# Optimization experiments

Measured on AMD Instinct MI355X. Metric: run time of the kernel, lower is better.

## Reference

```python
import jax, jax.numpy as jnp
import numpy as np

DIM = 512
HIDDEN = 4 * DIM
B, N = 512, 81
EPS = 1e-5


def _act_quant(x):
    # per-token int8 absmax quantization (BitNet b1.58)
    scale = 127.0 / jnp.clip(jnp.max(jnp.abs(x), axis=-1, keepdims=True), EPS, None)
    q = jnp.clip(jnp.round(x * scale), -128.0, 127.0) / scale
    return x + jax.lax.stop_gradient(q - x)  # STE


def _weight_quant(w):
    # per-tensor ternary quantization with mean-|w| scale
    scale = 1.0 / jnp.clip(jnp.mean(jnp.abs(w)), EPS, None)
    q = jnp.clip(jnp.round(w * scale), -1.0, 1.0) / scale
    return w + jax.lax.stop_gradient(q - w)  # STE


def bitlinear(x, w):
    # x: [..., in], w: [out, in] (torch Linear layout), no bias
    return _act_quant(x) @ _weight_quant(w).T


def setup_inputs() -> dict:
    key = jax.random.key(0)
    ks = jax.random.split(key, 8)
    def p(k, shape, fan_in):
        return jax.random.normal(k, shape, dtype=jnp.float32) * (fan_in ** -0.5)
    return {
        "x": jax.random.normal(ks[0], (B, N, DIM), dtype=jnp.float32),
        "y": jax.random.normal(ks[1], (B, N, DIM), dtype=jnp.float32),
        "s_prev": jax.random.normal(ks[2], (B, N, DIM), dtype=jnp.float32),
        "W_in": p(ks[3], (DIM, 3 * DIM), 3 * DIM),
        "W_fc1": p(ks[4], (HIDDEN, DIM), DIM),
        "W_fc2": p(ks[5], (DIM, HIDDEN), HIDDEN),
        "W_z": p(ks[6], (DIM, DIM), DIM),
        "W_mask": p(ks[7], (1, DIM), DIM),
    }


def reference(x, y, s_prev, W_in, W_fc1, W_fc2, W_z, W_mask):
    # inner: proj_in(cat) then residual BitMLP block(s)
    h = bitlinear(jnp.concatenate([x, y, s_prev], axis=-1), W_in)  # [B,N,DIM]
    h = h + bitlinear(jax.nn.gelu(bitlinear(h, W_fc1), approximate=False), W_fc2)
    # emit
    z = bitlinear(h, W_z)                      # [B,N,DIM]
    focus_mask = jax.nn.sigmoid(bitlinear(h, W_mask))  # [B,N,1]
    return (z, focus_mask)
```

## Files before the change

kernel.cpp:

```cpp
#include <hip/hip_runtime.h>
#include <math.h>

typedef unsigned short u16;
typedef unsigned int u32;
typedef __attribute__((ext_vector_type(8))) short short8;
typedef __attribute__((ext_vector_type(4))) float f32x4;

#define EPSQ 1e-5f
#define B_ROWS 41472
#define Z_ELEMS ((size_t)B_ROWS * 512)

__device__ __forceinline__ u16 f2b(float f) {
  u32 x = __float_as_uint(f);
  u32 r = (x + 0x7fffu + ((x >> 16) & 1u)) >> 16;
  return (u16)r;
}
__device__ __forceinline__ float blo(u32 v) { return __uint_as_float(v << 16); }
__device__ __forceinline__ float bhi(u32 v) { return __uint_as_float(v & 0xffff0000u); }
__device__ __forceinline__ u32 pack2(float a, float b) {
  return (u32)f2b(a) | ((u32)f2b(b) << 16);
}

__device__ __forceinline__ float wredMax(float v) {
#pragma unroll
  for (int off = 32; off; off >>= 1) v = fmaxf(v, __shfl_xor(v, off));
  return v;
}
__device__ __forceinline__ float wredSum(float v) {
#pragma unroll
  for (int off = 32; off; off >>= 1) v += __shfl_xor(v, off);
  return v;
}

__global__ __launch_bounds__(256) void wq_sum(const float* __restrict__ w, int n,
                                              float* __restrict__ sum) {
  float acc = 0.f;
  for (int i = blockIdx.x * blockDim.x + threadIdx.x; i < n; i += gridDim.x * blockDim.x)
    acc += fabsf(w[i]);
  acc = wredSum(acc);
  if ((threadIdx.x & 63) == 0) atomicAdd(sum, acc);
}

__global__ __launch_bounds__(256) void wq_quant(const float* __restrict__ w, int n,
                                                const float* __restrict__ sum,
                                                float* __restrict__ mout,
                                                u16* __restrict__ q) {
  const float m = fmaxf(sum[0] / (float)n, EPSQ);
  if (blockIdx.x == 0 && threadIdx.x == 0) mout[0] = m;
  const float s = 1.0f / m;
  for (int i = blockIdx.x * blockDim.x + threadIdx.x; i < n; i += gridDim.x * blockDim.x) {
    float t = rintf(w[i] * s);
    t = fminf(fmaxf(t, -1.f), 1.f);
    q[i] = f2b(t);
  }
}

__global__ __launch_bounds__(256) void aq_concat(const float* __restrict__ x,
                                                 const float* __restrict__ y,
                                                 const float* __restrict__ s,
                                                 u16* __restrict__ qx,
                                                 float* __restrict__ dsc, int row0) {
  const int r = blockIdx.x;
  const size_t R = (size_t)(row0 + r);
  const int t = threadIdx.x;
  float2 vx = *(const float2*)(x + R * 512 + t * 2);
  float2 vy = *(const float2*)(y + R * 512 + t * 2);
  float2 vs = *(const float2*)(s + R * 512 + t * 2);
  float mx = fmaxf(fmaxf(fabsf(vx.x), fabsf(vx.y)),
                   fmaxf(fmaxf(fabsf(vy.x), fabsf(vy.y)), fmaxf(fabsf(vs.x), fabsf(vs.y))));
  mx = wredMax(mx);
  __shared__ float red[4];
  if ((t & 63) == 0) red[t >> 6] = mx;
  __syncthreads();
  mx = fmaxf(fmaxf(red[0], red[1]), fmaxf(red[2], red[3]));
  const float m = fmaxf(mx, EPSQ);
  const float scq = 127.f / m;
  if (t == 0) dsc[r] = m * (1.f / 127.f);
  u16* qrow = qx + (size_t)r * 1536;
#define QZ(v) fminf(fmaxf(rintf((v) * scq), -128.f), 127.f)
  *(u32*)&qrow[t * 2] = pack2(QZ(vx.x), QZ(vx.y));
  *(u32*)&qrow[512 + t * 2] = pack2(QZ(vy.x), QZ(vy.y));
  *(u32*)&qrow[1024 + t * 2] = pack2(QZ(vs.x), QZ(vs.y));
#undef QZ
}

__global__ __launch_bounds__(256) void aq_row512(const float* __restrict__ src,
                                                 u16* __restrict__ q,
                                                 float* __restrict__ dsc) {
  const int row = blockIdx.x * 4 + (threadIdx.x >> 6);
  const int l = threadIdx.x & 63;
  const float* pr = src + (size_t)row * 512 + l * 8;
  float4 v0 = *(const float4*)pr;
  float4 v1 = *(const float4*)(pr + 4);
  float mx = fmaxf(fmaxf(fmaxf(fabsf(v0.x), fabsf(v0.y)), fmaxf(fabsf(v0.z), fabsf(v0.w))),
                   fmaxf(fmaxf(fabsf(v1.x), fabsf(v1.y)), fmaxf(fabsf(v1.z), fabsf(v1.w))));
  mx = wredMax(mx);
  const float m = fmaxf(mx, EPSQ);
  const float scq = 127.f / m;
  if (l == 0) dsc[row] = m * (1.f / 127.f);
#define QZ(v) fminf(fmaxf(rintf((v) * scq), -128.f), 127.f)
  uint4 o = make_uint4(pack2(QZ(v0.x), QZ(v0.y)), pack2(QZ(v0.z), QZ(v0.w)),
                       pack2(QZ(v1.x), QZ(v1.y)), pack2(QZ(v1.z), QZ(v1.w)));
#undef QZ
  *(uint4*)(q + (size_t)row * 512 + l * 8) = o;
}

__global__ __launch_bounds__(256) void aq_row2048(const u16* __restrict__ g,
                                                  u16* __restrict__ qg,
                                                  float* __restrict__ dsc) {
  const int r = blockIdx.x, t = threadIdx.x;
  uint4 raw = *(const uint4*)(g + (size_t)r * 2048 + t * 8);
  float f[8] = {blo(raw.x), bhi(raw.x), blo(raw.y), bhi(raw.y),
                blo(raw.z), bhi(raw.z), blo(raw.w), bhi(raw.w)};
  float mx = 0.f;
#pragma unroll
  for (int i = 0; i < 8; ++i) mx = fmaxf(mx, fabsf(f[i]));
  mx = wredMax(mx);
  __shared__ float red[4];
  if ((t & 63) == 0) red[t >> 6] = mx;
  __syncthreads();
  mx = fmaxf(fmaxf(red[0], red[1]), fmaxf(red[2], red[3]));
  const float m = fmaxf(mx, EPSQ);
  const float scq = 127.f / m;
  if (t == 0) dsc[r] = m * (1.f / 127.f);
#define QZ(v) fminf(fmaxf(rintf((v) * scq), -128.f), 127.f)
  uint4 o = make_uint4(pack2(QZ(f[0]), QZ(f[1])), pack2(QZ(f[2]), QZ(f[3])),
                       pack2(QZ(f[4]), QZ(f[5])), pack2(QZ(f[6]), QZ(f[7])));
#undef QZ
  *(uint4*)(qg + (size_t)r * 2048 + t * 8) = o;
}

__global__ __launch_bounds__(256) void bit_mask(const u16* __restrict__ qh,
                                                const float* __restrict__ dsc,
                                                const u16* __restrict__ qwm,
                                                const float* __restrict__ mWp,
                                                float* __restrict__ outp) {
  const int row = blockIdx.x * 4 + (threadIdx.x >> 6);
  const int l = threadIdx.x & 63;
  uint4 av = *(const uint4*)(qh + (size_t)row * 512 + l * 8);
  uint4 wv = *(const uint4*)(qwm + l * 8);
  float acc = blo(av.x) * blo(wv.x) + bhi(av.x) * bhi(wv.x) +
              blo(av.y) * blo(wv.y) + bhi(av.y) * bhi(wv.y) +
              blo(av.z) * blo(wv.z) + bhi(av.z) * bhi(wv.z) +
              blo(av.w) * blo(wv.w) + bhi(av.w) * bhi(wv.w);
  acc = wredSum(acc);
  if (l == 0) {
    float v = acc * dsc[row] * mWp[0];
    outp[row] = 1.f / (1.f + expf(-v));
  }
}

template <int EPI>
__global__ __launch_bounds__(256) void gemm_bt(const u16* __restrict__ A,
                                               const u16* __restrict__ Bw,
                                               const float* __restrict__ dA,
                                               const float* __restrict__ mWp,
                                               float* __restrict__ Cf,
                                               u16* __restrict__ Cb,
                                               int N, int K, int ldc) {
  __shared__ u16 lA[128 * 64];
  __shared__ u16 lB[128 * 64];
  const int tilesN = N >> 7;
  const int tm = blockIdx.x / tilesN, tn = blockIdx.x - tm * tilesN;
  const int t = threadIdx.x;
  const int w = t >> 6, l = t & 63;
  const int wr = w >> 1, wc = w & 1;
  const int lq = l >> 4, lr = l & 15;

  f32x4 zero = {0.f, 0.f, 0.f, 0.f};
  f32x4 acc[4][4];
#pragma unroll
  for (int m = 0; m < 4; ++m)
#pragma unroll
    for (int n = 0; n < 4; ++n) acc[m][n] = zero;

  const int srow = t >> 3;
  const int scb = t & 7;
  const size_t Abase = (size_t)(tm * 128 + srow) * K + scb * 8;
  const size_t Bbase = (size_t)(tn * 128 + srow) * K + scb * 8;

  for (int k0 = 0; k0 < K; k0 += 64) {
    int4 ra[4], rb[4];
#pragma unroll
    for (int r = 0; r < 4; ++r) {
      ra[r] = *(const int4*)(A + Abase + (size_t)r * 32 * K + k0);
      rb[r] = *(const int4*)(Bw + Bbase + (size_t)r * 32 * K + k0);
    }
    __syncthreads();
#pragma unroll
    for (int r = 0; r < 4; ++r) {
      int row = r * 32 + srow;
      *(int4*)&lA[row * 64 + ((scb ^ (row & 7)) << 3)] = ra[r];
      *(int4*)&lB[row * 64 + ((scb ^ (row & 7)) << 3)] = rb[r];
    }
    __syncthreads();
#pragma unroll
    for (int kk = 0; kk < 2; ++kk) {
      short8 av[4], bv[4];
#pragma unroll
      for (int m = 0; m < 4; ++m) {
        int row = wr * 64 + m * 16 + lr;
        av[m] = *(const short8*)&lA[row * 64 + (((kk * 4 + lq) ^ (row & 7)) << 3)];
      }
#pragma unroll
      for (int n = 0; n < 4; ++n) {
        int row = wc * 64 + n * 16 + lr;
        bv[n] = *(const short8*)&lB[row * 64 + (((kk * 4 + lq) ^ (row & 7)) << 3)];
      }
#pragma unroll
      for (int m = 0; m < 4; ++m)
#pragma unroll
        for (int n = 0; n < 4; ++n)
          acc[m][n] = __builtin_amdgcn_mfma_f32_16x16x32_bf16(av[m], bv[n], acc[m][n], 0, 0, 0);
    }
  }

  const float mw = mWp[0];
#pragma unroll
  for (int m = 0; m < 4; ++m) {
#pragma unroll
    for (int r = 0; r < 4; ++r) {
      const int row = tm * 128 + wr * 64 + m * 16 + lq * 4 + r;
      const float sc = dA[row] * mw;
#pragma unroll
      for (int n = 0; n < 4; ++n) {
        const int col = tn * 128 + wc * 64 + n * 16 + lr;
        float v = acc[m][n][r] * sc;
        if constexpr (EPI == 0) {
          Cf[(size_t)row * ldc + col] = v;
        } else if constexpr (EPI == 1) {
          v = 0.5f * v * (1.f + erff(v * 0.70710678f));
          Cb[(size_t)row * ldc + col] = f2b(v);
        } else {
          size_t ix = (size_t)row * ldc + col;
          Cf[ix] += v;
        }
      }
    }
  }
}

extern "C" void kernel_launch(void* const* d_in, const int* in_sizes, int n_in,
                              void* d_out, int out_size, void* d_ws, size_t ws_size,
                              hipStream_t stream) {
  const float* x = (const float*)d_in[0];
  const float* y = (const float*)d_in[1];
  const float* sp = (const float*)d_in[2];
  const float* Win = (const float*)d_in[3];
  const float* Wf1 = (const float*)d_in[4];
  const float* Wf2 = (const float*)d_in[5];
  const float* Wz = (const float*)d_in[6];
  const float* Wm = (const float*)d_in[7];
  float* out = (float*)d_out;

  const int TILES = B_ROWS / 128;
  char* p = (char*)d_ws;
  float* wsum = (float*)p; p += 256;
  float* mW = (float*)p; p += 256;
  u16* qWin = (u16*)p; p += (size_t)512 * 1536 * 2;
  u16* qWf1 = (u16*)p; p += (size_t)2048 * 512 * 2;
  u16* qWf2 = (u16*)p; p += (size_t)512 * 2048 * 2;
  u16* qWz = (u16*)p; p += (size_t)512 * 512 * 2;
  u16* qWm = (u16*)p; p += 1024;
  const size_t fixedB = (size_t)(p - (char*)d_ws);

  int Tc = 1;
  for (int nch = 1; nch <= TILES; ++nch) {
    int tc = (TILES + nch - 1) / nch;
    if (fixedB + (size_t)tc * 128 * 14352 + 1024 <= ws_size) { Tc = tc; break; }
  }
  const size_t McMax = (size_t)Tc * 128;
  u16* qx = (u16*)p; p += McMax * 1536 * 2;
  float* h = (float*)p; p += McMax * 512 * 4;
  u16* qh = (u16*)p; p += McMax * 512 * 2;
  u16* g = (u16*)p; p += McMax * 2048 * 2;
  u16* qg = (u16*)p; p += McMax * 2048 * 2;
  float* d1 = (float*)p; p += McMax * 4;
  float* d2 = (float*)p; p += McMax * 4;
  float* dgs = (float*)p; p += McMax * 4;
  float* d3 = (float*)p; p += McMax * 4;

  hipMemsetAsync(wsum, 0, 8 * sizeof(float), stream);
  wq_sum<<<64, 256, 0, stream>>>(Win, 512 * 1536, wsum + 0);
  wq_sum<<<64, 256, 0, stream>>>(Wf1, 2048 * 512, wsum + 1);
  wq_sum<<<64, 256, 0, stream>>>(Wf2, 512 * 2048, wsum + 2);
  wq_sum<<<64, 256, 0, stream>>>(Wz, 512 * 512, wsum + 3);
  wq_sum<<<8, 256, 0, stream>>>(Wm, 512, wsum + 4);
  wq_quant<<<64, 256, 0, stream>>>(Win, 512 * 1536, wsum + 0, mW + 0, qWin);
  wq_quant<<<64, 256, 0, stream>>>(Wf1, 2048 * 512, wsum + 1, mW + 1, qWf1);
  wq_quant<<<64, 256, 0, stream>>>(Wf2, 512 * 2048, wsum + 2, mW + 2, qWf2);
  wq_quant<<<16, 256, 0, stream>>>(Wz, 512 * 512, wsum + 3, mW + 3, qWz);
  wq_quant<<<2, 256, 0, stream>>>(Wm, 512, wsum + 4, mW + 4, qWm);

  for (int c0 = 0; c0 < TILES; c0 += Tc) {
    const int tiles = (TILES - c0 < Tc) ? (TILES - c0) : Tc;
    const int Mc = tiles * 128;
    const int row0 = c0 * 128;
    aq_concat<<<Mc, 256, 0, stream>>>(x, y, sp, qx, d1, row0);
    gemm_bt<0><<<tiles * 4, 256, 0, stream>>>(qx, qWin, d1, mW + 0, h, nullptr, 512, 1536, 512);
    aq_row512<<<Mc / 4, 256, 0, stream>>>(h, qh, d2);
    gemm_bt<1><<<tiles * 16, 256, 0, stream>>>(qh, qWf1, d2, mW + 1, nullptr, g, 2048, 512, 2048);
    aq_row2048<<<Mc, 256, 0, stream>>>(g, qg, dgs);
    gemm_bt<2><<<tiles * 4, 256, 0, stream>>>(qg, qWf2, dgs, mW + 2, h, nullptr, 512, 2048, 512);
    aq_row512<<<Mc / 4, 256, 0, stream>>>(h, qh, d3);
    gemm_bt<0><<<tiles * 4, 256, 0, stream>>>(qh, qWz, d3, mW + 3, out + (size_t)row0 * 512,
                                              nullptr, 512, 512, 512);
    bit_mask<<<Mc / 4, 256, 0, stream>>>(qh, d3, qWm, mW + 4, out + Z_ELEMS + row0);
  }
}
```

Before: 2.026 ms.

## Fuse activation quantization into GEMM epilogues with full-row N-tiles

Removes the standalone row-quantization kernels by adding a full-width (N=512) GEMM variant whose epilogue computes per-row absmax across waves and writes quantized bf16 activations plus scales directly. The fc1 GEMM epilogue now atomically accumulates per-row GELU absmax so the fc2 GEMM can quantize its A operand on load, eliminating the qg buffer and an extra read/write pass of the 2048-wide intermediate. The new 32x512 tile stages all of B through LDS each K step with 16 register loads per thread, which can hurt occupancy and latency hiding. aq_concat is also changed to 128 threads with float4 loads.

```diff
diff --git a/kernel.cpp b/kernel.cpp
--- a/kernel.cpp
+++ b/kernel.cpp
@@ -55,7 +55,7 @@
   }
 }
 
-__global__ __launch_bounds__(256) void aq_concat(const float* __restrict__ x,
+__global__ __launch_bounds__(128) void aq_concat(const float* __restrict__ x,
                                                  const float* __restrict__ y,
                                                  const float* __restrict__ s,
                                                  u16* __restrict__ qx,
@@ -63,71 +63,26 @@
   const int r = blockIdx.x;
   const size_t R = (size_t)(row0 + r);
   const int t = threadIdx.x;
-  float2 vx = *(const float2*)(x + R * 512 + t * 2);
-  float2 vy = *(const float2*)(y + R * 512 + t * 2);
-  float2 vs = *(const float2*)(s + R * 512 + t * 2);
-  float mx = fmaxf(fmaxf(fabsf(vx.x), fabsf(vx.y)),
-                   fmaxf(fmaxf(fabsf(vy.x), fabsf(vy.y)), fmaxf(fabsf(vs.x), fabsf(vs.y))));
+  float4 vx = *(const float4*)(x + R * 512 + t * 4);
+  float4 vy = *(const float4*)(y + R * 512 + t * 4);
+  float4 vs = *(const float4*)(s + R * 512 + t * 4);
+  float mx = fmaxf(fmaxf(fmaxf(fabsf(vx.x), fabsf(vx.y)), fmaxf(fabsf(vx.z), fabsf(vx.w))),
+            fmaxf(fmaxf(fmaxf(fabsf(vy.x), fabsf(vy.y)), fmaxf(fabsf(vy.z), fabsf(vy.w))),
+                  fmaxf(fmaxf(fabsf(vs.x), fabsf(vs.y)), fmaxf(fabsf(vs.z), fabsf(vs.w)))));
   mx = wredMax(mx);
-  __shared__ float red[4];
+  __shared__ float red[2];
   if ((t & 63) == 0) red[t >> 6] = mx;
   __syncthreads();
-  mx = fmaxf(fmaxf(red[0], red[1]), fmaxf(red[2], red[3]));
+  mx = fmaxf(red[0], red[1]);
   const float m = fmaxf(mx, EPSQ);
   const float scq = 127.f / m;
   if (t == 0) dsc[r] = m * (1.f / 127.f);
   u16* qrow = qx + (size_t)r * 1536;
 #define QZ(v) fminf(fmaxf(rintf((v) * scq), -128.f), 127.f)
-  *(u32*)&qrow[t * 2] = pack2(QZ(vx.x), QZ(vx.y));
-  *(u32*)&qrow[512 + t * 2] = pack2(QZ(vy.x), QZ(vy.y));
-  *(u32*)&qrow[1024 + t * 2] = pack2(QZ(vs.x), QZ(vs.y));
+  *(uint2*)&qrow[t * 4] = make_uint2(pack2(QZ(vx.x), QZ(vx.y)), pack2(QZ(vx.z), QZ(vx.w)));
+  *(uint2*)&qrow[512 + t * 4] = make_uint2(pack2(QZ(vy.x), QZ(vy.y)), pack2(QZ(vy.z), QZ(vy.w)));
+  *(uint2*)&qrow[1024 + t * 4] = make_uint2(pack2(QZ(vs.x), QZ(vs.y)), pack2(QZ(vs.z), QZ(vs.w)));
 #undef QZ
-}
-
-__global__ __launch_bounds__(256) void aq_row512(const float* __restrict__ src,
-                                                 u16* __restrict__ q,
-                                                 float* __restrict__ dsc) {
-  const int row = blockIdx.x * 4 + (threadIdx.x >> 6);
-  const int l = threadIdx.x & 63;
-  const float* pr = src + (size_t)row * 512 + l * 8;
-  float4 v0 = *(const float4*)pr;
-  float4 v1 = *(const float4*)(pr + 4);
-  float mx = fmaxf(fmaxf(fmaxf(fabsf(v0.x), fabsf(v0.y)), fmaxf(fabsf(v0.z), fabsf(v0.w))),
-                   fmaxf(fmaxf(fabsf(v1.x), fabsf(v1.y)), fmaxf(fabsf(v1.z), fabsf(v1.w))));
-  mx = wredMax(mx);
-  const float m = fmaxf(mx, EPSQ);
-  const float scq = 127.f / m;
-  if (l == 0) dsc[row] = m * (1.f / 127.f);
-#define QZ(v) fminf(fmaxf(rintf((v) * scq), -128.f), 127.f)
-  uint4 o = make_uint4(pack2(QZ(v0.x), QZ(v0.y)), pack2(QZ(v0.z), QZ(v0.w)),
-                       pack2(QZ(v1.x), QZ(v1.y)), pack2(QZ(v1.z), QZ(v1.w)));
-#undef QZ
-  *(uint4*)(q + (size_t)row * 512 + l * 8) = o;
-}
-
-__global__ __launch_bounds__(256) void aq_row2048(const u16* __restrict__ g,
-                                                  u16* __restrict__ qg,
-                                                  float* __restrict__ dsc) {
-  const int r = blockIdx.x, t = threadIdx.x;
-  uint4 raw = *(const uint4*)(g + (size_t)r * 2048 + t * 8);
-  float f[8] = {blo(raw.x), bhi(raw.x), blo(raw.y), bhi(raw.y),
-                blo(raw.z), bhi(raw.z), blo(raw.w), bhi(raw.w)};
-  float mx = 0.f;
-#pragma unroll
-  for (int i = 0; i < 8; ++i) mx = fmaxf(mx, fabsf(f[i]));
-  mx = wredMax(mx);
-  __shared__ float red[4];
-  if ((t & 63) == 0) red[t >> 6] = mx;
-  __syncthreads();
-  mx = fmaxf(fmaxf(red[0], red[1]), fmaxf(red[2], red[3]));
-  const float m = fmaxf(mx, EPSQ);
-  const float scq = 127.f / m;
-  if (t == 0) dsc[r] = m * (1.f / 127.f);
-#define QZ(v) fminf(fmaxf(rintf((v) * scq), -128.f), 127.f)
-  uint4 o = make_uint4(pack2(QZ(f[0]), QZ(f[1])), pack2(QZ(f[2]), QZ(f[3])),
-                       pack2(QZ(f[4]), QZ(f[5])), pack2(QZ(f[6]), QZ(f[7])));
-#undef QZ
-  *(uint4*)(qg + (size_t)r * 2048 + t * 8) = o;
 }
 
 __global__ __launch_bounds__(256) void bit_mask(const u16* __restrict__ qh,
@@ -157,6 +112,7 @@
                                                const float* __restrict__ mWp,
                                                float* __restrict__ Cf,
                                                u16* __restrict__ Cb,
+                                               float* __restrict__ rmaxG,
                                                int N, int K, int ldc) {
   __shared__ u16 lA[128 * 64];
   __shared__ u16 lB[128 * 64];
@@ -222,19 +178,147 @@
     for (int r = 0; r < 4; ++r) {
       const int row = tm * 128 + wr * 64 + m * 16 + lq * 4 + r;
       const float sc = dA[row] * mw;
+      float amax = 0.f;
 #pragma unroll
       for (int n = 0; n < 4; ++n) {
         const int col = tn * 128 + wc * 64 + n * 16 + lr;
         float v = acc[m][n][r] * sc;
         if constexpr (EPI == 0) {
           Cf[(size_t)row * ldc + col] = v;
-        } else if constexpr (EPI == 1) {
+        } else {
           v = 0.5f * v * (1.f + erff(v * 0.70710678f));
-          Cb[(size_t)row * ldc + col] = f2b(v);
-        } else {
-          size_t ix = (size_t)row * ldc + col;
-          Cf[ix] += v;
+          u16 b = f2b(v);
+          Cb[(size_t)row * ldc + col] = b;
+          amax = fmaxf(amax, fabsf(blo((u32)b)));
         }
+      }
+      if constexpr (EPI == 3) {
+#pragma unroll
+        for (int off = 1; off < 16; off <<= 1) amax = fmaxf(amax, __shfl_xor(amax, off));
+        if (lr == 0) atomicMax((int*)(rmaxG + row), __float_as_int(amax));
+      }
+    }
+  }
+}
+
+template <int AQ, int RESID>
+__global__ __launch_bounds__(256, 2) void gemm_fused(const u16* __restrict__ A,
+                                                     const u16* __restrict__ Bw,
+                                                     const float* __restrict__ dA,
+                                                     const float* __restrict__ mWp,
+                                                     float* __restrict__ h0,
+                                                     u16* __restrict__ qout,
+                                                     float* __restrict__ dscOut,
+                                                     int K) {
+  __shared__ u16 lA[32 * 64];
+  __shared__ u16 lB[512 * 64];
+  __shared__ float rmax[128];
+  const int tm = blockIdx.x;
+  const int t = threadIdx.x;
+  const int wc = t >> 6, l = t & 63;
+  const int lq = l >> 4, lr = l & 15;
+
+  f32x4 zero = {0.f, 0.f, 0.f, 0.f};
+  f32x4 acc[2][8];
+#pragma unroll
+  for (int m = 0; m < 2; ++m)
+#pragma unroll
+    for (int n = 0; n < 8; ++n) acc[m][n] = zero;
+
+  const int arow = t >> 3, acb = t & 7;
+  const size_t Abase = (size_t)(tm * 32 + arow) * K + acb * 8;
+  float scqA = 0.f;
+  if (AQ) scqA = 127.f / fmaxf(dA[tm * 32 + arow], EPSQ);
+
+  for (int k0 = 0; k0 < K; k0 += 64) {
+    int4 ra = *(const int4*)(A + Abase + k0);
+    int4 rb[16];
+#pragma unroll
+    for (int j = 0; j < 16; ++j) {
+      const int idx = j * 256 + t;
+      const int brow = idx >> 3, bcb = idx & 7;
+      rb[j] = *(const int4*)(Bw + (size_t)brow * K + k0 + bcb * 8);
+    }
+    if (AQ) {
+      u32* rw = (u32*)&ra;
+#pragma unroll
+      for (int j = 0; j < 4; ++j) {
+        float a0 = fminf(fmaxf(rintf(blo(rw[j]) * scqA), -128.f), 127.f);
+        float a1 = fminf(fmaxf(rintf(bhi(rw[j]) * scqA), -128.f), 127.f);
+        rw[j] = pack2(a0, a1);
+      }
+    }
+    __syncthreads();
+    *(int4*)&lA[arow * 64 + ((acb ^ (arow & 7)) << 3)] = ra;
+#pragma unroll
+    for (int j = 0; j < 16; ++j) {
+      const int idx = j * 256 + t;
+      const int brow = idx >> 3, bcb = idx & 7;
+      *(int4*)&lB[brow * 64 + ((bcb ^ (brow & 7)) << 3)] = rb[j];
+    }
+    __syncthreads();
+#pragma unroll
+    for (int kk = 0; kk < 2; ++kk) {
+      short8 av[2], bv[8];
+#pragma unroll
+      for (int m = 0; m < 2; ++m) {
+        int row = m * 16 + lr;
+        av[m] = *(const short8*)&lA[row * 64 + (((kk * 4 + lq) ^ (row & 7)) << 3)];
+      }
+#pragma unroll
+      for (int n = 0; n < 8; ++n) {
+        int row = wc * 128 + n * 16 + lr;
+        bv[n] = *(const short8*)&lB[row * 64 + (((kk * 4 + lq) ^ (row & 7)) << 3)];
+      }
+#pragma unroll
+      for (int m = 0; m < 2; ++m)
+#pragma unroll
+        for (int n = 0; n < 8; ++n)
+          acc[m][n] = __builtin_amdgcn_mfma_f32_16x16x32_bf16(av[m], bv[n], acc[m][n], 0, 0, 0);
+    }
+  }
+
+  const float mw = mWp[0];
+#pragma unroll
+  for (int m = 0; m < 2; ++m) {
+#pragma unroll
+    for (int rr = 0; rr < 4; ++rr) {
+      const int rloc = m * 16 + lq * 4 + rr;
+      const int grow = tm * 32 + rloc;
+      float da = AQ ? (fmaxf(dA[grow], EPSQ) * (1.f / 127.f)) : dA[grow];
+      const float sc = da * mw;
+      float amax = 0.f;
+#pragma unroll
+      for (int n = 0; n < 8; ++n) {
+        const int col = wc * 128 + n * 16 + lr;
+        float v = acc[m][n][rr] * sc;
+        if (RESID) v += h0[(size_t)grow * 512 + col];
+        else h0[(size_t)grow * 512 + col] = v;
+        acc[m][n][rr] = v;
+        amax = fmaxf(amax, fabsf(v));
+      }
+#pragma unroll
+      for (int off = 1; off < 16; off <<= 1) amax = fmaxf(amax, __shfl_xor(amax, off));
+      if (lr == 0) rmax[wc * 32 + rloc] = amax;
+    }
+  }
+  __syncthreads();
+#pragma unroll
+  for (int m = 0; m < 2; ++m) {
+#pragma unroll
+    for (int rr = 0; rr < 4; ++rr) {
+      const int rloc = m * 16 + lq * 4 + rr;
+      const int grow = tm * 32 + rloc;
+      float mx = fmaxf(fmaxf(rmax[rloc], rmax[32 + rloc]),
+                       fmaxf(rmax[64 + rloc], rmax[96 + rloc]));
+      const float m2 = fmaxf(mx, EPSQ);
+      const float sq = 127.f / m2;
+      if (wc == 0 && lr == 0) dscOut[grow] = m2 * (1.f / 127.f);
+#pragma unroll
+      for (int n = 0; n < 8; ++n) {
+        const int col = wc * 128 + n * 16 + lr;
+        float q = fminf(fmaxf(rintf(acc[m][n][rr] * sq), -128.f), 127.f);
+        qout[(size_t)grow * 512 + col] = f2b(q);
       }
     }
   }
@@ -267,18 +351,18 @@
   int Tc = 1;
   for (int nch = 1; nch <= TILES; ++nch) {
     int tc = (TILES + nch - 1) / nch;
-    if (fixedB + (size_t)tc * 128 * 14352 + 1024 <= ws_size) { Tc = tc; break; }
+    if (fixedB + (size_t)tc * 128 * 11280 + 4096 <= ws_size) { Tc = tc; break; }
   }
   const size_t McMax = (size_t)Tc * 128;
   u16* qx = (u16*)p; p += McMax * 1536 * 2;
-  float* h = (float*)p; p += McMax * 512 * 4;
+  float* d1 = (float*)p; p += McMax * 4;
+  float* h0 = (float*)p; p += McMax * 512 * 4;
   u16* qh = (u16*)p; p += McMax * 512 * 2;
+  float* dscH = (float*)p; p += McMax * 4;
   u16* g = (u16*)p; p += McMax * 2048 * 2;
-  u16* qg = (u16*)p; p += McMax * 2048 * 2;
-  float* d1 = (float*)p; p += McMax * 4;
-  float* d2 = (float*)p; p += McMax * 4;
-  float* dgs = (float*)p; p += McMax * 4;
-  float* d3 = (float*)p; p += McMax * 4;
+  float* rmG = (float*)p; p += McMax * 4;
+  u16* qh2 = (u16*)p; p += McMax * 512 * 2;
+  float* dsc2 = (float*)p; p += McMax * 4;
 
   hipMemsetAsync(wsum, 0, 8 * sizeof(float), stream);
   wq_sum<<<64, 256, 0, stream>>>(Win, 512 * 1536, wsum + 0);
@@ -296,15 +380,15 @@
     const int tiles = (TILES - c0 < Tc) ? (TILES - c0) : Tc;
     const int Mc = tiles * 128;
     const int row0 = c0 * 128;
-    aq_concat<<<Mc, 256, 0, stream>>>(x, y, sp, qx, d1, row0);
-    gemm_bt<0><<<tiles * 4, 256, 0, stream>>>(qx, qWin, d1, mW + 0, h, nullptr, 512, 1536, 512);
-    aq_row512<<<Mc / 4, 256, 0, stream>>>(h, qh, d2);
-    gemm_bt<1><<<tiles * 16, 256, 0, stream>>>(qh, qWf1, d2, mW + 1, nullptr, g, 2048, 512, 2048);
-    aq_row2048<<<Mc, 256, 0, stream>>>(g, qg, dgs);
-    gemm_bt<2><<<tiles * 4, 256, 0, stream>>>(qg, qWf2, dgs, mW + 2, h, nullptr, 512, 2048, 512);
-    aq_row512<<<Mc / 4, 256, 0, stream>>>(h, qh, d3);
-    gemm_bt<0><<<tiles * 4, 256, 0, stream>>>(qh, qWz, d3, mW + 3, out + (size_t)row0 * 512,
-                                              nullptr, 512, 512, 512);
-    bit_mask<<<Mc / 4, 256, 0, stream>>>(qh, d3, qWm, mW + 4, out + Z_ELEMS + row0);
-  }
-}
+    hipMemsetAsync(rmG, 0, (size_t)Mc * 4, stream);
+    aq_concat<<<Mc, 128, 0, stream>>>(x, y, sp, qx, d1, row0);
+    gemm_fused<0, 0><<<Mc / 32, 256, 0, stream>>>(qx, qWin, d1, mW + 0, h0, qh, dscH, 1536);
+    gemm_bt<3><<<tiles * 16, 256, 0, stream>>>(qh, qWf1, dscH, mW + 1, nullptr, g, rmG,
+                                               2048, 512, 2048);
+    gemm_fused<1, 1><<<Mc / 32, 256, 0, stream>>>(g, qWf2, rmG, mW + 2, h0, qh2, dsc2, 2048);
+    gemm_bt<0><<<tiles * 4, 256, 0, stream>>>(qh2, qWz, dsc2, mW + 3,
+                                              out + (size_t)row0 * 512, nullptr, nullptr,
+                                              512, 512, 512);
+    bit_mask<<<Mc / 4, 256, 0, stream>>>(qh2, dsc2, qWm, mW + 4, out + Z_ELEMS + row0);
+  }
+}
```

Result: slower. 2.608 ms (+28.7%).

## Fuse GELU row absmax into fc1 epilogue and quantize A on load in fc2

Applied to the files above, without the earlier changes.

The fc1 GEMM epilogue now computes a per-row absmax of the bf16 GELU output and merges it across tiles with atomicMax. The fc2 GEMM quantizes its A tile in registers at load time using that absmax. This removes the separate aq_row2048 pass and the qg buffer, which saves a full read and write of the 2048-wide intermediate. Other changes: the concat quantizer uses 128 threads with float4 loads, the chunk search starts at 6 chunks for smaller working sets, and a per-chunk memset of the absmax buffer is added. The cost is extra quantization arithmetic in the fc2 K loop, which is repeated for every N tile, plus atomic contention.

```diff
diff --git a/kernel.cpp b/kernel.cpp
--- a/kernel.cpp
+++ b/kernel.cpp
@@ -55,7 +55,7 @@
   }
 }
 
-__global__ __launch_bounds__(256) void aq_concat(const float* __restrict__ x,
+__global__ __launch_bounds__(128) void aq_concat(const float* __restrict__ x,
                                                  const float* __restrict__ y,
                                                  const float* __restrict__ s,
                                                  u16* __restrict__ qx,
@@ -63,24 +63,25 @@
   const int r = blockIdx.x;
   const size_t R = (size_t)(row0 + r);
   const int t = threadIdx.x;
-  float2 vx = *(const float2*)(x + R * 512 + t * 2);
-  float2 vy = *(const float2*)(y + R * 512 + t * 2);
-  float2 vs = *(const float2*)(s + R * 512 + t * 2);
-  float mx = fmaxf(fmaxf(fabsf(vx.x), fabsf(vx.y)),
-                   fmaxf(fmaxf(fabsf(vy.x), fabsf(vy.y)), fmaxf(fabsf(vs.x), fabsf(vs.y))));
+  float4 vx = *(const float4*)(x + R * 512 + t * 4);
+  float4 vy = *(const float4*)(y + R * 512 + t * 4);
+  float4 vs = *(const float4*)(s + R * 512 + t * 4);
+  float mx = fmaxf(fmaxf(fmaxf(fabsf(vx.x), fabsf(vx.y)), fmaxf(fabsf(vx.z), fabsf(vx.w))),
+            fmaxf(fmaxf(fmaxf(fabsf(vy.x), fabsf(vy.y)), fmaxf(fabsf(vy.z), fabsf(vy.w))),
+                  fmaxf(fmaxf(fabsf(vs.x), fabsf(vs.y)), fmaxf(fabsf(vs.z), fabsf(vs.w)))));
   mx = wredMax(mx);
-  __shared__ float red[4];
+  __shared__ float red[2];
   if ((t & 63) == 0) red[t >> 6] = mx;
   __syncthreads();
-  mx = fmaxf(fmaxf(red[0], red[1]), fmaxf(red[2], red[3]));
+  mx = fmaxf(red[0], red[1]);
   const float m = fmaxf(mx, EPSQ);
   const float scq = 127.f / m;
   if (t == 0) dsc[r] = m * (1.f / 127.f);
   u16* qrow = qx + (size_t)r * 1536;
 #define QZ(v) fminf(fmaxf(rintf((v) * scq), -128.f), 127.f)
-  *(u32*)&qrow[t * 2] = pack2(QZ(vx.x), QZ(vx.y));
-  *(u32*)&qrow[512 + t * 2] = pack2(QZ(vy.x), QZ(vy.y));
-  *(u32*)&qrow[1024 + t * 2] = pack2(QZ(vs.x), QZ(vs.y));
+  *(uint2*)&qrow[t * 4] = make_uint2(pack2(QZ(vx.x), QZ(vx.y)), pack2(QZ(vx.z), QZ(vx.w)));
+  *(uint2*)&qrow[512 + t * 4] = make_uint2(pack2(QZ(vy.x), QZ(vy.y)), pack2(QZ(vy.z), QZ(vy.w)));
+  *(uint2*)&qrow[1024 + t * 4] = make_uint2(pack2(QZ(vs.x), QZ(vs.y)), pack2(QZ(vs.z), QZ(vs.w)));
 #undef QZ
 }
 
@@ -105,31 +106,6 @@
   *(uint4*)(q + (size_t)row * 512 + l * 8) = o;
 }
 
-__global__ __launch_bounds__(256) void aq_row2048(const u16* __restrict__ g,
-                                                  u16* __restrict__ qg,
-                                                  float* __restrict__ dsc) {
-  const int r = blockIdx.x, t = threadIdx.x;
-  uint4 raw = *(const uint4*)(g + (size_t)r * 2048 + t * 8);
-  float f[8] = {blo(raw.x), bhi(raw.x), blo(raw.y), bhi(raw.y),
-                blo(raw.z), bhi(raw.z), blo(raw.w), bhi(raw.w)};
-  float mx = 0.f;
-#pragma unroll
-  for (int i = 0; i < 8; ++i) mx = fmaxf(mx, fabsf(f[i]));
-  mx = wredMax(mx);
-  __shared__ float red[4];
-  if ((t & 63) == 0) red[t >> 6] = mx;
-  __syncthreads();
-  mx = fmaxf(fmaxf(red[0], red[1]), fmaxf(red[2], red[3]));
-  const float m = fmaxf(mx, EPSQ);
-  const float scq = 127.f / m;
-  if (t == 0) dsc[r] = m * (1.f / 127.f);
-#define QZ(v) fminf(fmaxf(rintf((v) * scq), -128.f), 127.f)
-  uint4 o = make_uint4(pack2(QZ(f[0]), QZ(f[1])), pack2(QZ(f[2]), QZ(f[3])),
-                       pack2(QZ(f[4]), QZ(f[5])), pack2(QZ(f[6]), QZ(f[7])));
-#undef QZ
-  *(uint4*)(qg + (size_t)r * 2048 + t * 8) = o;
-}
-
 __global__ __launch_bounds__(256) void bit_mask(const u16* __restrict__ qh,
                                                 const float* __restrict__ dsc,
                                                 const u16* __restrict__ qwm,
@@ -150,13 +126,14 @@
   }
 }
 
-template <int EPI>
+template <int EPI, int AQ>
 __global__ __launch_bounds__(256) void gemm_bt(const u16* __restrict__ A,
                                                const u16* __restrict__ Bw,
                                                const float* __restrict__ dA,
                                                const float* __restrict__ mWp,
                                                float* __restrict__ Cf,
                                                u16* __restrict__ Cb,
+                                               float* __restrict__ rmaxG,
                                                int N, int K, int ldc) {
   __shared__ u16 lA[128 * 64];
   __shared__ u16 lB[128 * 64];
@@ -179,12 +156,31 @@
   const size_t Abase = (size_t)(tm * 128 + srow) * K + scb * 8;
   const size_t Bbase = (size_t)(tn * 128 + srow) * K + scb * 8;
 
+  float scq[4];
+  if (AQ) {
+#pragma unroll
+    for (int r = 0; r < 4; ++r)
+      scq[r] = 127.f / fmaxf(dA[tm * 128 + r * 32 + srow], EPSQ);
+  }
+
   for (int k0 = 0; k0 < K; k0 += 64) {
     int4 ra[4], rb[4];
 #pragma unroll
     for (int r = 0; r < 4; ++r) {
       ra[r] = *(const int4*)(A + Abase + (size_t)r * 32 * K + k0);
       rb[r] = *(const int4*)(Bw + Bbase + (size_t)r * 32 * K + k0);
+    }
+    if (AQ) {
+#pragma unroll
+      for (int r = 0; r < 4; ++r) {
+        u32* rw = (u32*)&ra[r];
+#pragma unroll
+        for (int j = 0; j < 4; ++j) {
+          float a0 = fminf(fmaxf(rintf(blo(rw[j]) * scq[r]), -128.f), 127.f);
+          float a1 = fminf(fmaxf(rintf(bhi(rw[j]) * scq[r]), -128.f), 127.f);
+          rw[j] = pack2(a0, a1);
+        }
+      }
     }
     __syncthreads();
 #pragma unroll
@@ -221,20 +217,29 @@
 #pragma unroll
     for (int r = 0; r < 4; ++r) {
       const int row = tm * 128 + wr * 64 + m * 16 + lq * 4 + r;
-      const float sc = dA[row] * mw;
+      const float da = AQ ? (fmaxf(dA[row], EPSQ) * (1.f / 127.f)) : dA[row];
+      const float sc = da * mw;
+      float amax = 0.f;
 #pragma unroll
       for (int n = 0; n < 4; ++n) {
         const int col = tn * 128 + wc * 64 + n * 16 + lr;
         float v = acc[m][n][r] * sc;
         if constexpr (EPI == 0) {
           Cf[(size_t)row * ldc + col] = v;
-        } else if constexpr (EPI == 1) {
-          v = 0.5f * v * (1.f + erff(v * 0.70710678f));
-          Cb[(size_t)row * ldc + col] = f2b(v);
-        } else {
+        } else if constexpr (EPI == 2) {
           size_t ix = (size_t)row * ldc + col;
           Cf[ix] += v;
+        } else {
+          v = 0.5f * v * (1.f + erff(v * 0.70710678f));
+          u16 b = f2b(v);
+          Cb[(size_t)row * ldc + col] = b;
+          amax = fmaxf(amax, fabsf(blo((u32)b)));
         }
+      }
+      if constexpr (EPI == 3) {
+#pragma unroll
+        for (int off = 1; off < 16; off <<= 1) amax = fmaxf(amax, __shfl_xor(amax, off));
+        if (lr == 0) atomicMax((int*)(rmaxG + row), __float_as_int(amax));
       }
     }
   }
@@ -265,19 +270,19 @@
   const size_t fixedB = (size_t)(p - (char*)d_ws);
 
   int Tc = 1;
-  for (int nch = 1; nch <= TILES; ++nch) {
+  for (int nch = 6; nch <= TILES; ++nch) {
     int tc = (TILES + nch - 1) / nch;
-    if (fixedB + (size_t)tc * 128 * 14352 + 1024 <= ws_size) { Tc = tc; break; }
+    if (fixedB + (size_t)tc * 128 * 11280 + 4096 <= ws_size) { Tc = tc; break; }
   }
   const size_t McMax = (size_t)Tc * 128;
   u16* qx = (u16*)p; p += McMax * 1536 * 2;
+  float* d1 = (float*)p; p += McMax * 4;
   float* h = (float*)p; p += McMax * 512 * 4;
   u16* qh = (u16*)p; p += McMax * 512 * 2;
+  float* d2 = (float*)p; p += McMax * 4;
   u16* g = (u16*)p; p += McMax * 2048 * 2;
-  u16* qg = (u16*)p; p += McMax * 2048 * 2;
-  float* d1 = (float*)p; p += McMax * 4;
-  float* d2 = (float*)p; p += McMax * 4;
-  float* dgs = (float*)p; p += McMax * 4;
+  float* rmG = (float*)p; p += McMax * 4;
+  u16* qh2 = (u16*)p; p += McMax * 512 * 2;
   float* d3 = (float*)p; p += McMax * 4;
 
   hipMemsetAsync(wsum, 0, 8 * sizeof(float), stream);
@@ -296,15 +301,19 @@
     const int tiles = (TILES - c0 < Tc) ? (TILES - c0) : Tc;
     const int Mc = tiles * 128;
     const int row0 = c0 * 128;
-    aq_concat<<<Mc, 256, 0, stream>>>(x, y, sp, qx, d1, row0);
-    gemm_bt<0><<<tiles * 4, 256, 0, stream>>>(qx, qWin, d1, mW + 0, h, nullptr, 512, 1536, 512);
+    hipMemsetAsync(rmG, 0, (size_t)Mc * 4, stream);
+    aq_concat<<<Mc, 128, 0, stream>>>(x, y, sp, qx, d1, row0);
+    gemm_bt<0, 0><<<tiles * 4, 256, 0, stream>>>(qx, qWin, d1, mW + 0, h, nullptr, nullptr,
+                                                 512, 1536, 512);
     aq_row512<<<Mc / 4, 256, 0, stream>>>(h, qh, d2);
-    gemm_bt<1><<<tiles * 16, 256, 0, stream>>>(qh, qWf1, d2, mW + 1, nullptr, g, 2048, 512, 2048);
-    aq_row2048<<<Mc, 256, 0, stream>>>(g, qg, dgs);
-    gemm_bt<2><<<tiles * 4, 256, 0, stream>>>(qg, qWf2, dgs, mW + 2, h, nullptr, 512, 2048, 512);
-    aq_row512<<<Mc / 4, 256, 0, stream>>>(h, qh, d3);
-    gemm_bt<0><<<tiles * 4, 256, 0, stream>>>(qh, qWz, d3, mW + 3, out + (size_t)row0 * 512,
-                                              nullptr, 512, 512, 512);
-    bit_mask<<<Mc / 4, 256, 0, stream>>>(qh, d3, qWm, mW + 4, out + Z_ELEMS + row0);
-  }
-}
+    gemm_bt<3, 0><<<tiles * 16, 256, 0, stream>>>(qh, qWf1, d2, mW + 1, nullptr, g, rmG,
+                                                  2048, 512, 2048);
+    gemm_bt<2, 1><<<tiles * 4, 256, 0, stream>>>(g, qWf2, rmG, mW + 2, h, nullptr, nullptr,
+                                                 512, 2048, 512);
+    aq_row512<<<Mc / 4, 256, 0, stream>>>(h, qh2, d3);
+    gemm_bt<0, 0><<<tiles * 4, 256, 0, stream>>>(qh2, qWz, d3, mW + 3,
+                                                 out + (size_t)row0 * 512, nullptr, nullptr,
+                                                 512, 512, 512);
+    bit_mask<<<Mc / 4, 256, 0, stream>>>(qh2, d3, qWm, mW + 4, out + Z_ELEMS + row0);
+  }
+}
```

Result: no change. 2.050 ms (+1.2%).
